# Kernel optimization log

Hardware: AMD Instinct MI355X
Metric: run time of the kernel (lower is better)

Reference implementation:

```python
import jax, jax.numpy as jnp
import numpy as np

EPS = 1e-5
SLOPE = 0.01  # torch LeakyReLU default


def _leaky(x):
    return jnp.where(x > 0, x, SLOPE * x)


def _layernorm(x, g, b):
    mu = jnp.mean(x, axis=-1, keepdims=True)
    var = jnp.var(x, axis=-1, keepdims=True)
    return (x - mu) * jax.lax.rsqrt(var + EPS) * g + b


def setup_inputs() -> dict:
    key = jax.random.key(0)
    B, N, E, L = 1, 512, 256, 64
    D = E + L  # 320
    ks = jax.random.split(key, 16)
    p = {}
    p["robot_embedding"] = jax.random.normal(ks[0], (B, N, E), jnp.float32)
    p["object_embedding"] = jax.random.normal(ks[1], (B, N, E), jnp.float32)
    p["language_emb"] = jax.random.normal(ks[2], (B, L), jnp.float32)
    # MLPKernel params: Linear(2D->D) + LN + LeakyReLU, Linear(D->D) + LN + LeakyReLU, Linear(D->1)
    p["W1"] = jax.random.normal(ks[3], (2 * D, D), jnp.float32) * 0.02
    p["b1"] = jnp.zeros((D,), jnp.float32)
    p["g1"] = jnp.ones((D,), jnp.float32)
    p["be1"] = jnp.zeros((D,), jnp.float32)
    p["W2"] = jax.random.normal(ks[4], (D, D), jnp.float32) * 0.02
    p["b2"] = jnp.zeros((D,), jnp.float32)
    p["g2"] = jnp.ones((D,), jnp.float32)
    p["be2"] = jnp.zeros((D,), jnp.float32)
    p["W3"] = jax.random.normal(ks[5], (D, 1), jnp.float32) * 0.02
    p["b3"] = jnp.zeros((1,), jnp.float32)
    return p


def _forward(robot_embedding, object_embedding, language_emb,
             W1, b1, g1, be1, W2, b2, g2, be2, W3, b3):
    B, N, E = robot_embedding.shape
    # use_language=True path: z = language_emb, broadcast over N and concat
    z = jnp.broadcast_to(language_emb[:, None, :], (B, N, language_emb.shape[-1]))
    Phi_A = jnp.concatenate([robot_embedding, z], axis=-1)   # [B,N,D]
    Phi_B = jnp.concatenate([object_embedding, z], axis=-1)  # [B,N,D]
    D = Phi_A.shape[-1]
    # Pairwise concat [B,N,N,2D] == kernel(Phi_A_r, Phi_B_r) on the full grid.
    # Equivalent to the block_computing loop (same math, different tiling).
    fA = jnp.broadcast_to(Phi_A[:, :, None, :], (B, N, N, D))
    fB = jnp.broadcast_to(Phi_B[:, None, :, :], (B, N, N, D))
    feat = jnp.concatenate([fA, fB], axis=-1)  # [B,N,N,2D]
    h = _leaky(_layernorm(feat @ W1 + b1, g1, be1))
    h = _leaky(_layernorm(h @ W2 + b2, g2, be2))
    dro = jnp.abs((h @ W3 + b3)[..., 0])  # [B,N,N]
    return dro


def reference(robot_embedding, object_embedding, language_emb,
              W1, b1, g1, be1, W2, b2, g2, be2, W3, b3):
    dro = _forward(robot_embedding, object_embedding, language_emb,
                   W1, b1, g1, be1, W2, b2, g2, be2, W3, b3)
    # outputs = {'dro': dro, 'mu': None, 'logvar': None} -> return dro
    return dro
```

## Files before the change

kernel.cpp:

```cpp
#include <hip/hip_runtime.h>
#include <hip/hip_bf16.h>

#define LN_EPS 1e-5f
#define SLOPE 0.01f

typedef short bf16x8 __attribute__((ext_vector_type(8)));
typedef float f32x4 __attribute__((ext_vector_type(4)));

__global__ __launch_bounds__(320) void prep_kernel(
    const float* __restrict__ robot, const float* __restrict__ object,
    const float* __restrict__ lang, const float* __restrict__ W1,
    const float* __restrict__ b1, const float* __restrict__ W2,
    float* __restrict__ U, float* __restrict__ V,
    __hip_bfloat16* __restrict__ Ub, __hip_bfloat16* __restrict__ Vb,
    float* __restrict__ stats, __hip_bfloat16* __restrict__ W2F)
{
  __shared__ float red[5][2];
  __shared__ float tile[32][33];
  const int bx = blockIdx.x;
  const int tid = threadIdx.x;

  if (bx < 1024) {
    const int i = bx >> 1;
    const int isV = bx & 1;
    const int d = tid;
    const float* __restrict__ src   = isV ? object : robot;
    const float* __restrict__ Wbase = W1 + (isV ? 320 * 320 : 0);

    float a0 = 0.f, a1 = 0.f, a2 = 0.f, a3 = 0.f;
#pragma unroll 4
    for (int k = 0; k < 256; k += 4) {
      a0 = fmaf(src[i * 256 + k + 0], Wbase[(k + 0) * 320 + d], a0);
      a1 = fmaf(src[i * 256 + k + 1], Wbase[(k + 1) * 320 + d], a1);
      a2 = fmaf(src[i * 256 + k + 2], Wbase[(k + 2) * 320 + d], a2);
      a3 = fmaf(src[i * 256 + k + 3], Wbase[(k + 3) * 320 + d], a3);
    }
#pragma unroll 4
    for (int l = 0; l < 64; l += 4) {
      a0 = fmaf(lang[l + 0], Wbase[(256 + l + 0) * 320 + d], a0);
      a1 = fmaf(lang[l + 1], Wbase[(256 + l + 1) * 320 + d], a1);
      a2 = fmaf(lang[l + 2], Wbase[(256 + l + 2) * 320 + d], a2);
      a3 = fmaf(lang[l + 3], Wbase[(256 + l + 3) * 320 + d], a3);
    }
    float acc = (a0 + a1) + (a2 + a3);
    if (isV) acc += b1[d];

    (isV ? V : U)[i * 320 + d] = acc;
    (isV ? Vb : Ub)[i * 320 + d] = __float2bfloat16(acc);

    float s = acc, q = acc * acc;
#pragma unroll
    for (int m = 1; m < 64; m <<= 1) {
      s += __shfl_xor(s, m);
      q += __shfl_xor(q, m);
    }
    const int w = d >> 6, lane = d & 63;
    if (lane == 0) { red[w][0] = s; red[w][1] = q; }
    __syncthreads();
    if (d == 0) {
      float s0 = 0.f, q0 = 0.f;
      for (int t = 0; t < 5; ++t) { s0 += red[t][0]; q0 += red[t][1]; }
      stats[isV * 1024 + i] = s0;
      stats[isV * 1024 + 512 + i] = q0;
    }
  } else {
    const int t = bx - 1024;
    const int d0 = (t % 10) * 32;
    const int kk = t / 10;
    if (tid < 256) {
      const int tx = tid & 31, ty = tid >> 5;
#pragma unroll
      for (int r = 0; r < 32; r += 8)
        tile[ty + r][tx] = W2[((kk * 32) + ty + r) * 320 + d0 + tx];
    }
    __syncthreads();
    if (tid < 256) {
      const int fl   = tid >> 7;
      const int l    = (tid >> 1) & 63;
      const int half = tid & 1;
      const int frag = (d0 >> 4) + fl;
      __hip_bfloat16* dst = W2F + ((kk * 20 + frag) * 512) + l * 8 + half * 4;
#pragma unroll
      for (int e = 0; e < 4; ++e)
        dst[e] = __float2bfloat16(tile[(l >> 4) * 8 + half * 4 + e]
                                      [fl * 16 + (l & 15)]);
    }
  }
}

__global__ __launch_bounds__(256, 3) void fused_main(
    const float* __restrict__ U, const float* __restrict__ V,
    const __hip_bfloat16* __restrict__ Ub, const __hip_bfloat16* __restrict__ Vb,
    const __hip_bfloat16* __restrict__ W2F, const float* __restrict__ stats,
    const float* __restrict__ g1, const float* __restrict__ be1,
    const float* __restrict__ b2, const float* __restrict__ g2,
    const float* __restrict__ be2, const float* __restrict__ W3,
    const float* __restrict__ b3, float* __restrict__ out)
{
  __shared__ __align__(16) __hip_bfloat16 h1[64 * 320];
  __shared__ __align__(16) float U_lds[320], g1_lds[320], be1_lds[320];
  __shared__ float dt_lds[64];
  __shared__ float part[64][4][2];
  __shared__ float pdot[64][4];

  const int i   = blockIdx.x;
  const int j0  = blockIdx.y * 64;
  const int tid = threadIdx.x;
  const int lane = tid & 63;
  const int w    = tid >> 6;
  const int r16  = lane & 15;
  const int g    = lane >> 4;
  const int row  = tid >> 2;
  const int seg  = tid & 3;

  for (int t = tid; t < 320; t += 256) {
    U_lds[t]   = U[i * 320 + t];
    g1_lds[t]  = g1[t];
    be1_lds[t] = be1[t];
  }

  {
    const __hip_bfloat16* __restrict__ Ubrow = Ub + i * 320 + g * 8;
    const __hip_bfloat16* __restrict__ Vbrow =
        Vb + (size_t)(j0 + w * 16 + r16) * 320 + g * 8;
    f32x4 accd = (f32x4){0.f, 0.f, 0.f, 0.f};
#pragma unroll
    for (int kk = 0; kk < 10; ++kk) {
      const bf16x8 da = *(const bf16x8*)(Ubrow + kk * 32);
      const bf16x8 db = *(const bf16x8*)(Vbrow + kk * 32);
      accd = __builtin_amdgcn_mfma_f32_16x16x32_bf16(da, db, accd, 0, 0, 0);
    }
    if (lane < 16)
      dt_lds[w * 16 + lane] = accd[0];
  }

  const float* __restrict__ Vrow = V + (j0 + row) * 320 + seg * 80;
  f32x4 vreg[20];
#pragma unroll
  for (int m = 0; m < 20; ++m)
    vreg[m] = *(const f32x4*)(Vrow + m * 4);
  const float sVr = stats[1024 + j0 + row];
  const float qVr = stats[1536 + j0 + row];
  const float sU  = stats[i], qU = stats[512 + i];

  const int wc = w;
  const __hip_bfloat16* __restrict__ Bf = W2F + (size_t)(wc * 5) * 512 + lane * 8;
  bf16x8 bbuf[2][5];
#pragma unroll
  for (int nf = 0; nf < 5; ++nf)
    bbuf[0][nf] = *(const bf16x8*)(Bf + nf * 512);

  __syncthreads();

  const float dt   = dt_lds[row];
  const float mu   = (sU + sVr) * (1.f / 320.f);
  const float var  = (qU + 2.f * dt + qVr) * (1.f / 320.f) - mu * mu;
  const float rs   = rsqrtf(var + LN_EPS);
  const float murs = mu * rs;
  {
    const unsigned swz  = (unsigned)((row & 7) << 4);
    const unsigned base = (unsigned)row * 640u + (unsigned)seg * 160u;
#pragma unroll
    for (int m = 0; m < 10; ++m) {
      const int d = seg * 80 + m * 8;
      const f32x4 va = vreg[2 * m];
      const f32x4 vb = vreg[2 * m + 1];
      const f32x4 ua = *(const f32x4*)&U_lds[d];
      const f32x4 ub = *(const f32x4*)&U_lds[d + 4];
      const f32x4 ga = *(const f32x4*)&g1_lds[d];
      const f32x4 gb = *(const f32x4*)&g1_lds[d + 4];
      const f32x4 ea = *(const f32x4*)&be1_lds[d];
      const f32x4 eb = *(const f32x4*)&be1_lds[d + 4];
      union { bf16x8 v; __hip_bfloat16 e[8]; } pk;
#pragma unroll
      for (int e = 0; e < 4; ++e) {
        const float x = ua[e] + va[e];
        float hv = fmaf(fmaf(x, rs, -murs), ga[e], ea[e]);
        hv = fmaxf(hv, SLOPE * hv);
        pk.e[e] = __float2bfloat16(hv);
      }
#pragma unroll
      for (int e = 0; e < 4; ++e) {
        const float x = ub[e] + vb[e];
        float hv = fmaf(fmaf(x, rs, -murs), gb[e], eb[e]);
        hv = fmaxf(hv, SLOPE * hv);
        pk.e[4 + e] = __float2bfloat16(hv);
      }
      *(bf16x8*)((char*)h1 + ((base + (unsigned)m * 16u) ^ swz)) = pk.v;
    }
  }
  __syncthreads();

  f32x4 acc[4][5];
#pragma unroll
  for (int mf = 0; mf < 4; ++mf)
#pragma unroll
    for (int nf = 0; nf < 5; ++nf)
      acc[mf][nf] = (f32x4){0.f, 0.f, 0.f, 0.f};

  const unsigned swzA = (unsigned)((r16 & 7) << 4);
  unsigned arow[4];
#pragma unroll
  for (int mf = 0; mf < 4; ++mf)
    arow[mf] = (unsigned)(mf * 16 + r16) * 640u;

#pragma unroll
  for (int kk = 0; kk < 10; ++kk) {
    const int cur = kk & 1, nxt = cur ^ 1;
    if (kk < 9) {
#pragma unroll
      for (int nf = 0; nf < 5; ++nf)
        bbuf[nxt][nf] = *(const bf16x8*)(Bf + ((kk + 1) * 20 + nf) * 512);
    }
    const unsigned k2 = (unsigned)((kk * 32 + g * 8) * 2);
    bf16x8 a[4];
#pragma unroll
    for (int mf = 0; mf < 4; ++mf)
      a[mf] = *(const bf16x8*)((const char*)h1 + ((arow[mf] + k2) ^ swzA));
#pragma unroll
    for (int nf = 0; nf < 5; ++nf)
#pragma unroll
      for (int mf = 0; mf < 4; ++mf)
        acc[mf][nf] = __builtin_amdgcn_mfma_f32_16x16x32_bf16(
            a[mf], bbuf[cur][nf], acc[mf][nf], 0, 0, 0);
  }

  float b2c[5], g2c[5], be2c[5], w3c[5];
#pragma unroll
  for (int nf = 0; nf < 5; ++nf) {
    const int col = wc * 80 + nf * 16 + r16;
    b2c[nf]  = b2[col];
    g2c[nf]  = g2[col];
    be2c[nf] = be2[col];
    w3c[nf]  = W3[col];
  }
#pragma unroll
  for (int nf = 0; nf < 5; ++nf)
#pragma unroll
    for (int mf = 0; mf < 4; ++mf)
#pragma unroll
      for (int r = 0; r < 4; ++r)
        acc[mf][nf][r] += b2c[nf];

#pragma unroll
  for (int mf = 0; mf < 4; ++mf) {
#pragma unroll
    for (int r = 0; r < 4; ++r) {
      float s = 0.f, q = 0.f;
#pragma unroll
      for (int nf = 0; nf < 5; ++nf) {
        const float v = acc[mf][nf][r];
        s += v;
        q = fmaf(v, v, q);
      }
#pragma unroll
      for (int m = 1; m < 16; m <<= 1) {
        s += __shfl_xor(s, m);
        q += __shfl_xor(q, m);
      }
      if (r16 == 0) {
        const int rw = mf * 16 + g * 4 + r;
        part[rw][wc][0] = s;
        part[rw][wc][1] = q;
      }
    }
  }
  __syncthreads();

#pragma unroll
  for (int mf = 0; mf < 4; ++mf) {
#pragma unroll
    for (int r = 0; r < 4; ++r) {
      const int rw = mf * 16 + g * 4 + r;
      const float s = part[rw][0][0] + part[rw][1][0] +
                      part[rw][2][0] + part[rw][3][0];
      const float q = part[rw][0][1] + part[rw][1][1] +
                      part[rw][2][1] + part[rw][3][1];
      const float mu2  = s * (1.f / 320.f);
      const float var2 = q * (1.f / 320.f) - mu2 * mu2;
      const float rs2  = rsqrtf(var2 + LN_EPS);
      const float murs2 = mu2 * rs2;
      float dsum = 0.f;
#pragma unroll
      for (int nf = 0; nf < 5; ++nf) {
        float v = fmaf(fmaf(acc[mf][nf][r], rs2, -murs2), g2c[nf], be2c[nf]);
        v = fmaxf(v, SLOPE * v);
        dsum = fmaf(v, w3c[nf], dsum);
      }
#pragma unroll
      for (int m = 1; m < 16; m <<= 1)
        dsum += __shfl_xor(dsum, m);
      if (r16 == 0)
        pdot[rw][wc] = dsum;
    }
  }
  __syncthreads();

  if (tid < 64) {
    const float tot = pdot[tid][0] + pdot[tid][1] + pdot[tid][2] +
                      pdot[tid][3] + b3[0];
    out[i * 512 + j0 + tid] = fabsf(tot);
  }
}

extern "C" void kernel_launch(void* const* d_in, const int* in_sizes, int n_in,
                              void* d_out, int out_size, void* d_ws, size_t ws_size,
                              hipStream_t stream) {
  const float* robot  = (const float*)d_in[0];
  const float* object = (const float*)d_in[1];
  const float* lang   = (const float*)d_in[2];
  const float* W1  = (const float*)d_in[3];
  const float* b1  = (const float*)d_in[4];
  const float* g1  = (const float*)d_in[5];
  const float* be1 = (const float*)d_in[6];
  const float* W2  = (const float*)d_in[7];
  const float* b2  = (const float*)d_in[8];
  const float* g2  = (const float*)d_in[9];
  const float* be2 = (const float*)d_in[10];
  const float* W3  = (const float*)d_in[11];
  const float* b3  = (const float*)d_in[12];
  float* out = (float*)d_out;

  float* U     = (float*)d_ws;
  float* V     = U + 512 * 320;
  float* stats = V + 512 * 320;
  __hip_bfloat16* W2F = (__hip_bfloat16*)(stats + 2048);
  __hip_bfloat16* Ub  = W2F + 320 * 320;
  __hip_bfloat16* Vb  = Ub + 512 * 320;

  prep_kernel<<<1124, 320, 0, stream>>>(robot, object, lang, W1, b1, W2,
                                        U, V, Ub, Vb, stats, W2F);
  fused_main<<<dim3(512, 8), 256, 0, stream>>>(U, V, Ub, Vb, W2F, stats,
                                               g1, be1, b2, g2, be2, W3, b3,
                                               out);
}
```

Measured before the change: 218.0 us.

## Batch prep rows, pre-fragment V bf16, and replace shuffle reductions with LDS

The prep kernel now computes four rows per block so each W1 load is reused four times, and the language contribution is computed once and added to all four rows. The bf16 copy of V is written in MFMA fragment order, so the dot-product MFMA in the main kernel reads contiguous fragments. In the main kernel, the LayerNorm-2 statistic and W3 dot-product reductions switch from 16-lane shuffle trees to LDS scratch (reusing the h1 buffer) plus cooperative sums. This costs extra barriers and shared-memory traffic in exchange for fewer cross-lane operations.

```diff
diff --git a/kernel.cpp b/kernel.cpp
--- a/kernel.cpp
+++ b/kernel.cpp
@@ -12,59 +12,73 @@
     const float* __restrict__ lang, const float* __restrict__ W1,
     const float* __restrict__ b1, const float* __restrict__ W2,
     float* __restrict__ U, float* __restrict__ V,
-    __hip_bfloat16* __restrict__ Ub, __hip_bfloat16* __restrict__ Vb,
+    __hip_bfloat16* __restrict__ Ub, __hip_bfloat16* __restrict__ VbF,
     float* __restrict__ stats, __hip_bfloat16* __restrict__ W2F)
 {
-  __shared__ float red[5][2];
+  __shared__ float sh[4][321];
   __shared__ float tile[32][33];
   const int bx = blockIdx.x;
   const int tid = threadIdx.x;
 
-  if (bx < 1024) {
-    const int i = bx >> 1;
+  if (bx < 256) {
+    const int i0  = (bx >> 1) * 4;
     const int isV = bx & 1;
-    const int d = tid;
+    const int d   = tid;
     const float* __restrict__ src   = isV ? object : robot;
     const float* __restrict__ Wbase = W1 + (isV ? 320 * 320 : 0);
 
     float a0 = 0.f, a1 = 0.f, a2 = 0.f, a3 = 0.f;
 #pragma unroll 4
-    for (int k = 0; k < 256; k += 4) {
-      a0 = fmaf(src[i * 256 + k + 0], Wbase[(k + 0) * 320 + d], a0);
-      a1 = fmaf(src[i * 256 + k + 1], Wbase[(k + 1) * 320 + d], a1);
-      a2 = fmaf(src[i * 256 + k + 2], Wbase[(k + 2) * 320 + d], a2);
-      a3 = fmaf(src[i * 256 + k + 3], Wbase[(k + 3) * 320 + d], a3);
-    }
+    for (int k = 0; k < 256; ++k) {
+      const float w1v = Wbase[k * 320 + d];
+      a0 = fmaf(src[(i0 + 0) * 256 + k], w1v, a0);
+      a1 = fmaf(src[(i0 + 1) * 256 + k], w1v, a1);
+      a2 = fmaf(src[(i0 + 2) * 256 + k], w1v, a2);
+      a3 = fmaf(src[(i0 + 3) * 256 + k], w1v, a3);
+    }
+    float la = 0.f;
 #pragma unroll 4
-    for (int l = 0; l < 64; l += 4) {
-      a0 = fmaf(lang[l + 0], Wbase[(256 + l + 0) * 320 + d], a0);
-      a1 = fmaf(lang[l + 1], Wbase[(256 + l + 1) * 320 + d], a1);
-      a2 = fmaf(lang[l + 2], Wbase[(256 + l + 2) * 320 + d], a2);
-      a3 = fmaf(lang[l + 3], Wbase[(256 + l + 3) * 320 + d], a3);
-    }
-    float acc = (a0 + a1) + (a2 + a3);
-    if (isV) acc += b1[d];
-
-    (isV ? V : U)[i * 320 + d] = acc;
-    (isV ? Vb : Ub)[i * 320 + d] = __float2bfloat16(acc);
-
-    float s = acc, q = acc * acc;
-#pragma unroll
-    for (int m = 1; m < 64; m <<= 1) {
-      s += __shfl_xor(s, m);
-      q += __shfl_xor(q, m);
-    }
-    const int w = d >> 6, lane = d & 63;
-    if (lane == 0) { red[w][0] = s; red[w][1] = q; }
+    for (int l = 0; l < 64; ++l)
+      la = fmaf(lang[l], Wbase[(256 + l) * 320 + d], la);
+    if (isV) la += b1[d];
+    a0 += la; a1 += la; a2 += la; a3 += la;
+
+    const float av[4] = {a0, a1, a2, a3};
+#pragma unroll
+    for (int r = 0; r < 4; ++r) {
+      const int i = i0 + r;
+      (isV ? V : U)[i * 320 + d] = av[r];
+      if (!isV) {
+        Ub[i * 320 + d] = __float2bfloat16(av[r]);
+      } else {
+        const int jt = i >> 4, kkv = d >> 5, gv = (d >> 3) & 3, ev = d & 7;
+        VbF[((jt * 10 + kkv) * 512) + (gv * 16 + (i & 15)) * 8 + ev] =
+            __float2bfloat16(av[r]);
+      }
+      sh[r][d] = av[r];
+    }
     __syncthreads();
-    if (d == 0) {
-      float s0 = 0.f, q0 = 0.f;
-      for (int t = 0; t < 5; ++t) { s0 += red[t][0]; q0 += red[t][1]; }
-      stats[isV * 1024 + i] = s0;
-      stats[isV * 1024 + 512 + i] = q0;
+    const int w = tid >> 6, lane = tid & 63;
+    if (w < 4) {
+      float s = 0.f, q = 0.f;
+#pragma unroll
+      for (int c = 0; c < 5; ++c) {
+        const float v = sh[w][lane + c * 64];
+        s += v;
+        q = fmaf(v, v, q);
+      }
+#pragma unroll
+      for (int m = 1; m < 64; m <<= 1) {
+        s += __shfl_xor(s, m);
+        q += __shfl_xor(q, m);
+      }
+      if (lane == 0) {
+        stats[isV * 1024 + i0 + w] = s;
+        stats[isV * 1024 + 512 + i0 + w] = q;
+      }
     }
   } else {
-    const int t = bx - 1024;
+    const int t = bx - 256;
     const int d0 = (t % 10) * 32;
     const int kk = t / 10;
     if (tid < 256) {
@@ -90,7 +104,7 @@
 
 __global__ __launch_bounds__(256, 3) void fused_main(
     const float* __restrict__ U, const float* __restrict__ V,
-    const __hip_bfloat16* __restrict__ Ub, const __hip_bfloat16* __restrict__ Vb,
+    const __hip_bfloat16* __restrict__ Ub, const __hip_bfloat16* __restrict__ VbF,
     const __hip_bfloat16* __restrict__ W2F, const float* __restrict__ stats,
     const float* __restrict__ g1, const float* __restrict__ be1,
     const float* __restrict__ b2, const float* __restrict__ g2,
@@ -100,8 +114,8 @@
   __shared__ __align__(16) __hip_bfloat16 h1[64 * 320];
   __shared__ __align__(16) float U_lds[320], g1_lds[320], be1_lds[320];
   __shared__ float dt_lds[64];
-  __shared__ float part[64][4][2];
-  __shared__ float pdot[64][4];
+  __shared__ float s4[64][5], q4[64][5], e4[64][5];
+  __shared__ float rsm[64][2];
 
   const int i   = blockIdx.x;
   const int j0  = blockIdx.y * 64;
@@ -121,13 +135,13 @@
 
   {
     const __hip_bfloat16* __restrict__ Ubrow = Ub + i * 320 + g * 8;
-    const __hip_bfloat16* __restrict__ Vbrow =
-        Vb + (size_t)(j0 + w * 16 + r16) * 320 + g * 8;
+    const __hip_bfloat16* __restrict__ VbFp =
+        VbF + ((size_t)((j0 >> 4) + w) * 10) * 512 + lane * 8;
     f32x4 accd = (f32x4){0.f, 0.f, 0.f, 0.f};
 #pragma unroll
     for (int kk = 0; kk < 10; ++kk) {
       const bf16x8 da = *(const bf16x8*)(Ubrow + kk * 32);
-      const bf16x8 db = *(const bf16x8*)(Vbrow + kk * 32);
+      const bf16x8 db = *(const bf16x8*)(VbFp + kk * 512);
       accd = __builtin_amdgcn_mfma_f32_16x16x32_bf16(da, db, accd, 0, 0, 0);
     }
     if (lane < 16)
@@ -242,6 +256,9 @@
       for (int r = 0; r < 4; ++r)
         acc[mf][nf][r] += b2c[nf];
 
+  float* scr = (float*)h1;
+  __syncthreads();
+
 #pragma unroll
   for (int mf = 0; mf < 4; ++mf) {
 #pragma unroll
@@ -253,17 +270,34 @@
         s += v;
         q = fmaf(v, v, q);
       }
-#pragma unroll
-      for (int m = 1; m < 16; m <<= 1) {
-        s += __shfl_xor(s, m);
-        q += __shfl_xor(q, m);
-      }
-      if (r16 == 0) {
-        const int rw = mf * 16 + g * 4 + r;
-        part[rw][wc][0] = s;
-        part[rw][wc][1] = q;
-      }
-    }
+      const int rw = mf * 16 + g * 4 + r;
+      scr[rw * 65 + wc * 16 + r16] = s;
+      scr[4160 + rw * 65 + wc * 16 + r16] = q;
+    }
+  }
+  __syncthreads();
+
+  {
+    const int r = tid & 63, qq = tid >> 6;
+    float s = 0.f, q = 0.f;
+#pragma unroll
+    for (int k = 0; k < 16; ++k) {
+      s += scr[r * 65 + qq * 16 + k];
+      q += scr[4160 + r * 65 + qq * 16 + k];
+    }
+    s4[r][qq] = s;
+    q4[r][qq] = q;
+  }
+  __syncthreads();
+
+  if (tid < 64) {
+    const float s = s4[tid][0] + s4[tid][1] + s4[tid][2] + s4[tid][3];
+    const float q = q4[tid][0] + q4[tid][1] + q4[tid][2] + q4[tid][3];
+    const float mu2  = s * (1.f / 320.f);
+    const float var2 = q * (1.f / 320.f) - mu2 * mu2;
+    const float rs2  = rsqrtf(var2 + LN_EPS);
+    rsm[tid][0] = rs2;
+    rsm[tid][1] = mu2 * rs2;
   }
   __syncthreads();
 
@@ -272,14 +306,7 @@
 #pragma unroll
     for (int r = 0; r < 4; ++r) {
       const int rw = mf * 16 + g * 4 + r;
-      const float s = part[rw][0][0] + part[rw][1][0] +
-                      part[rw][2][0] + part[rw][3][0];
-      const float q = part[rw][0][1] + part[rw][1][1] +
-                      part[rw][2][1] + part[rw][3][1];
-      const float mu2  = s * (1.f / 320.f);
-      const float var2 = q * (1.f / 320.f) - mu2 * mu2;
-      const float rs2  = rsqrtf(var2 + LN_EPS);
-      const float murs2 = mu2 * rs2;
+      const float rs2 = rsm[rw][0], murs2 = rsm[rw][1];
       float dsum = 0.f;
 #pragma unroll
       for (int nf = 0; nf < 5; ++nf) {
@@ -287,18 +314,23 @@
         v = fmaxf(v, SLOPE * v);
         dsum = fmaf(v, w3c[nf], dsum);
       }
-#pragma unroll
-      for (int m = 1; m < 16; m <<= 1)
-        dsum += __shfl_xor(dsum, m);
-      if (r16 == 0)
-        pdot[rw][wc] = dsum;
-    }
+      scr[rw * 65 + wc * 16 + r16] = dsum;
+    }
+  }
+  __syncthreads();
+
+  {
+    const int r = tid & 63, qq = tid >> 6;
+    float s = 0.f;
+#pragma unroll
+    for (int k = 0; k < 16; ++k)
+      s += scr[r * 65 + qq * 16 + k];
+    e4[r][qq] = s;
   }
   __syncthreads();
 
   if (tid < 64) {
-    const float tot = pdot[tid][0] + pdot[tid][1] + pdot[tid][2] +
-                      pdot[tid][3] + b3[0];
+    const float tot = e4[tid][0] + e4[tid][1] + e4[tid][2] + e4[tid][3] + b3[0];
     out[i * 512 + j0 + tid] = fabsf(tot);
   }
 }
@@ -326,11 +358,11 @@
   float* stats = V + 512 * 320;
   __hip_bfloat16* W2F = (__hip_bfloat16*)(stats + 2048);
   __hip_bfloat16* Ub  = W2F + 320 * 320;
-  __hip_bfloat16* Vb  = Ub + 512 * 320;
-
-  prep_kernel<<<1124, 320, 0, stream>>>(robot, object, lang, W1, b1, W2,
-                                        U, V, Ub, Vb, stats, W2F);
-  fused_main<<<dim3(512, 8), 256, 0, stream>>>(U, V, Ub, Vb, W2F, stats,
+  __hip_bfloat16* VbF = Ub + 512 * 320;
+
+  prep_kernel<<<356, 320, 0, stream>>>(robot, object, lang, W1, b1, W2,
+                                       U, V, Ub, VbF, stats, W2F);
+  fused_main<<<dim3(512, 8), 256, 0, stream>>>(U, V, Ub, VbF, W2F, stats,
                                                g1, be1, b2, g2, be2, W3, b3,
                                                out);
 }
```

Result: faster. 193.2 us (-11.3%).
